# Optimization experiments

Hardware: AMD Instinct MI355X
Metric: run time of the kernel (lower is better)

The kernel has to match this reference:

```python
import jax, jax.numpy as jnp
import numpy as np

BUCKET = 64      # bucket_size
N_HASHES = 8
HEADS = 8
EMB = 256
DH = EMB // HEADS  # 32, per-head dim
SELF_ATTN_VAL = -5e4  # TOKEN_SELF_ATTN_VALUE in reformer-pytorch


def haar_dwt2_per(x):
    # one-level 2D haar DWT, periodization mode. x: [B,C,H,W] (H,W even)
    B, C, H, W = x.shape
    x = x.reshape(B, C, H // 2, 2, W // 2, 2)
    a = x[:, :, :, 0, :, 0]
    b = x[:, :, :, 0, :, 1]
    c = x[:, :, :, 1, :, 0]
    d = x[:, :, :, 1, :, 1]
    ll = (a + b + c + d) * 0.5
    lh = (a - b + c - d) * 0.5  # high-pass along W
    hl = (a + b - c - d) * 0.5  # high-pass along H
    hh = (a - b - c + d) * 0.5
    return ll, lh, hl, hh


def maxpool_3s2p1(x):
    # MaxPool2d(kernel=3, stride=2, padding=1)
    return jax.lax.reduce_window(x, -jnp.inf, jax.lax.max,
                                 (1, 1, 3, 3), (1, 1, 2, 2),
                                 ((0, 0), (0, 0), (1, 1), (1, 1)))


def _look_one_back(a):
    # concat each chunk with the previous chunk (wrap-around), along axis 2
    prev = jnp.concatenate([a[:, -1:], a[:, :-1]], axis=1)
    return jnp.concatenate([a, prev], axis=2)


def lsh_attention(qk, v, rotations):
    # qk, v: [bh, t, d]; rotations: [d, n_hashes, n_buckets//2]
    bh, t, d = qk.shape
    n_buckets = t // BUCKET
    # --- hash ---
    rotated = jnp.einsum('btf,fhi->bhti', qk, rotations)        # [bh,nh,t,nb/2]
    rotated = jnp.concatenate([rotated, -rotated], axis=-1)     # [bh,nh,t,nb]
    buckets = jnp.argmax(rotated, axis=-1)                      # [bh,nh,t]
    offsets = (jnp.arange(N_HASHES) * n_buckets)[None, :, None]
    buckets = (buckets + offsets).reshape(bh, -1)               # [bh, nh*t]
    # --- sort tokens by bucket ---
    ticker = jnp.arange(N_HASHES * t)
    bat = t * buckets + (ticker % t)[None, :]
    sticker = jnp.argsort(bat, axis=-1)                         # stable sort
    undo = jnp.argsort(sticker, axis=-1)
    st = sticker % t
    sqk = jnp.take_along_axis(qk, st[..., None], axis=1)
    sv = jnp.take_along_axis(v, st[..., None], axis=1)
    nc = N_HASHES * n_buckets
    bq_t = st.reshape(bh, nc, BUCKET)
    bqk = sqk.reshape(bh, nc, BUCKET, d)
    bv = sv.reshape(bh, nc, BUCKET, d)
    bq = bqk
    norm = jnp.linalg.norm(bqk, axis=-1, keepdims=True)
    bk = bqk / jnp.maximum(norm, 1e-6)                          # make_unit_length
    bk = _look_one_back(bk)
    bv = _look_one_back(bv)
    bkv_t = _look_one_back(bq_t[..., None])[..., 0]
    # --- bucketed attention ---
    dots = jnp.einsum('bnie,bnje->bnij', bq, bk) * (d ** -0.5)  # [bh,nc,64,128]
    self_mask = bq_t[:, :, :, None] == bkv_t[:, :, None, :]
    dots = jnp.where(self_mask, SELF_ATTN_VAL, dots)
    lse = jax.scipy.special.logsumexp(dots, axis=-1, keepdims=True)
    probs = jnp.exp(dots - lse)
    bo = jnp.einsum('bnij,bnje->bnie', probs, bv)
    so = bo.reshape(bh, -1, d)
    slog = lse.reshape(bh, -1)
    # --- unsort and combine hash rounds ---
    o = jnp.take_along_axis(so, undo[..., None], axis=1).reshape(bh, N_HASHES, t, d)
    logits = jnp.take_along_axis(slog, undo, axis=1).reshape(bh, N_HASHES, t, 1)
    w = jnp.exp(logits - jax.scipy.special.logsumexp(logits, axis=1, keepdims=True))
    return jnp.sum(o * w, axis=1)                               # [bh, t, d]


def setup_inputs() -> dict:
    key = jax.random.key(0)
    ks = jax.random.split(key, 6)
    B, C, H, W = 16, 128, 32, 32
    scale = 1.0 / np.sqrt(EMB)
    return {
        'x': jax.random.normal(ks[0], (B, C, H, W), dtype=jnp.float32),
        'w_qk': jax.random.normal(ks[1], (EMB, EMB), dtype=jnp.float32) * scale,
        'w_v': jax.random.normal(ks[2], (EMB, EMB), dtype=jnp.float32) * scale,
        'w_out': jax.random.normal(ks[3], (EMB, EMB), dtype=jnp.float32) * scale,
        'b_out': jnp.zeros((EMB,), dtype=jnp.float32),
        'rotations': jax.random.normal(ks[4], (DH, N_HASHES, 5), dtype=jnp.float32),
    }


def reference(x, w_qk, w_v, w_out, b_out, rotations):
    B = x.shape[0]
    x_spatial = maxpool_3s2p1(x)                      # [B,C,16,16]
    ll, lh, hl, hh = haar_dwt2_per(x)                 # each [B,C,16,16]
    xc = jnp.concatenate([x_spatial, ll, lh, hl, hh], axis=1)  # [B,5C,16,16]
    _, N, Hh, Ww = xc.shape
    tokens = xc.reshape(B, N, Hh * Ww)                # [B, 640, 256]
    qk = tokens @ w_qk
    v = tokens @ w_v
    qkh = qk.reshape(B, N, HEADS, DH).transpose(0, 2, 1, 3).reshape(B * HEADS, N, DH)
    vh = v.reshape(B, N, HEADS, DH).transpose(0, 2, 1, 3).reshape(B * HEADS, N, DH)
    o = lsh_attention(qkh, vh, rotations)
    o = o.reshape(B, HEADS, N, DH).transpose(0, 2, 1, 3).reshape(B, N, EMB)
    out = o @ w_out + b_out
    return out.reshape(B, N, Hh, Ww)
```

## Files before the change

kernel.cpp:

```cpp
#include <hip/hip_runtime.h>
#include <math.h>

#define B_     16
#define CIN_   128
#define NTOK_  640
#define PSP_   256
#define EMB_   256
#define HEADS_ 8
#define DH_    32
#define BH_    128
#define NH_    8
#define NBK_   10
#define NC_    80
#define TOTROWS_ 10240
#define SORTLEN_ 5120
#define VSTRIDE 136

typedef __attribute__((ext_vector_type(8))) short short8;
typedef __attribute__((ext_vector_type(4))) short short4v;
typedef __attribute__((ext_vector_type(4))) float f32x4;

__device__ __forceinline__ unsigned bf16r(float f) {
  return (__float_as_uint(f) + 0x8000u) >> 16;
}

__device__ __forceinline__ unsigned cvt_pk_bf16(float a, float b) {
  unsigned r;
  asm("v_cvt_pk_bf16_f32 %0, %1, %2" : "=v"(r) : "v"(a), "v"(b));
  return r;
}

__global__ __launch_bounds__(256) void k_tokens(const float* __restrict__ x,
                                                float* __restrict__ tok,
                                                const float* __restrict__ wv,
                                                const float* __restrict__ wo,
                                                unsigned short* __restrict__ wtv,
                                                unsigned short* __restrict__ wto) {
  if (blockIdx.x < 256) {
    int idx = blockIdx.x * 256 + threadIdx.x;
    int n = idx >> 8, k = idx & 255;
    wtv[idx] = (unsigned short)bf16r(wv[k * 256 + n]);
    wto[idx] = (unsigned short)bf16r(wo[k * 256 + n]);
  }
  int tid = blockIdx.x * 256 + threadIdx.x;
  int p  = tid & 255;
  int bc = tid >> 8;
  int i = p >> 4, j = p & 15;
  const float* xp = x + (size_t)bc * 1024;
  int r0 = i * 2, c0 = j * 2;

  float mx = -3.4e38f;
  #pragma unroll
  for (int dr = -1; dr <= 1; dr++) {
    int r = r0 + dr;
    if (r < 0 || r >= 32) continue;
    #pragma unroll
    for (int dc = -1; dc <= 1; dc++) {
      int cc = c0 + dc;
      if (cc < 0 || cc >= 32) continue;
      mx = fmaxf(mx, xp[r * 32 + cc]);
    }
  }
  float a  = xp[r0 * 32 + c0];
  float bv = xp[r0 * 32 + c0 + 1];
  float cv = xp[(r0 + 1) * 32 + c0];
  float dv = xp[(r0 + 1) * 32 + c0 + 1];
  float ll = (a + bv + cv + dv) * 0.5f;
  float lh = (a - bv + cv - dv) * 0.5f;
  float hl = (a + bv - cv - dv) * 0.5f;
  float hh = (a - bv - cv + dv) * 0.5f;

  int b = bc >> 7, c = bc & 127;
  float* tb = tok + (size_t)b * NTOK_ * PSP_ + p;
  tb[(size_t)(c      ) * PSP_] = mx;
  tb[(size_t)(c + 128) * PSP_] = ll;
  tb[(size_t)(c + 256) * PSP_] = lh;
  tb[(size_t)(c + 384) * PSP_] = hl;
  tb[(size_t)(c + 512) * PSP_] = hh;
}

__global__ __launch_bounds__(256) void k_gemm_qv(const float* __restrict__ A,
                                                 const float* __restrict__ Wq,
                                                 const unsigned short* __restrict__ WTv,
                                                 float* __restrict__ C,
                                                 unsigned short* __restrict__ Cb,
                                                 unsigned short* __restrict__ Cv) {
  __shared__ float As[64][68];
  __shared__ float Bs[64][64];
  int tid = threadIdx.x;

  if (blockIdx.x < 640) {
    int bx = blockIdx.x;
    int row0 = (bx >> 2) * 64, col0 = (bx & 3) * 64;
    int tx = tid & 15, ty = tid >> 4;
    float acc[4][4] = {};

    int lrow = tid >> 2, lkq = tid & 3;
    int bkr = tid >> 4, bcq = tid & 15;

    for (int k0 = 0; k0 < 256; k0 += 64) {
      float4 va[4], vb4[4];
      #pragma unroll
      for (int i = 0; i < 4; i++) {
        va[i]  = *(const float4*)(&A[(size_t)(row0 + lrow) * 256 + k0 + i * 16 + 4 * lkq]);
        vb4[i] = *(const float4*)(&Wq[(size_t)(k0 + i * 16 + bkr) * 256 + col0 + 4 * bcq]);
      }
      __syncthreads();
      #pragma unroll
      for (int i = 0; i < 4; i++) {
        As[i * 16 + 4 * lkq + 0][lrow] = va[i].x;
        As[i * 16 + 4 * lkq + 1][lrow] = va[i].y;
        As[i * 16 + 4 * lkq + 2][lrow] = va[i].z;
        As[i * 16 + 4 * lkq + 3][lrow] = va[i].w;
        *(float4*)(&Bs[i * 16 + bkr][4 * bcq]) = vb4[i];
      }
      __syncthreads();
      #pragma unroll
      for (int k = 0; k < 64; k++) {
        const float4 b4 = *(const float4*)(&Bs[k][4 * tx]);
        const float4 a4 = *(const float4*)(&As[k][4 * ty]);
        float ar[4] = {a4.x, a4.y, a4.z, a4.w};
        #pragma unroll
        for (int r = 0; r < 4; r++) {
          acc[r][0] += ar[r] * b4.x; acc[r][1] += ar[r] * b4.y;
          acc[r][2] += ar[r] * b4.z; acc[r][3] += ar[r] * b4.w;
        }
      }
    }
    #pragma unroll
    for (int r = 0; r < 4; r++) {
      float4 o;
      o.x = acc[r][0]; o.y = acc[r][1]; o.z = acc[r][2]; o.w = acc[r][3];
      size_t off = (size_t)(row0 + 4 * ty + r) * 256 + col0 + 4 * tx;
      *(float4*)(&C[off]) = o;
      uint2 ub;
      ub.x = bf16r(o.x) | (bf16r(o.y) << 16);
      ub.y = bf16r(o.z) | (bf16r(o.w) << 16);
      *(uint2*)(&Cb[off]) = ub;
    }
  } else {
    int vbk = blockIdx.x - 640;
    int wid = tid >> 6, lane = tid & 63;
    int lane15 = lane & 15, quad = lane >> 4;
    int row0 = (vbk >> 1) * 64 + wid * 16;
    int col0 = (vbk & 1) * 128;

    short8 fa[8];
    const float* arow = A + (size_t)(row0 + lane15) * 256;
    #pragma unroll
    for (int kc = 0; kc < 8; kc++) {
      float4 x0 = *(const float4*)(arow + kc * 32 + quad * 8);
      float4 x1 = *(const float4*)(arow + kc * 32 + quad * 8 + 4);
      short8 f;
      f[0] = (short)bf16r(x0.x); f[1] = (short)bf16r(x0.y);
      f[2] = (short)bf16r(x0.z); f[3] = (short)bf16r(x0.w);
      f[4] = (short)bf16r(x1.x); f[5] = (short)bf16r(x1.y);
      f[6] = (short)bf16r(x1.z); f[7] = (short)bf16r(x1.w);
      fa[kc] = f;
    }
    #pragma unroll
    for (int nt = 0; nt < 8; nt++) {
      int col = col0 + nt * 16 + lane15;
      f32x4 acc = {0.f, 0.f, 0.f, 0.f};
      const unsigned short* wrow = WTv + (size_t)col * 256;
      #pragma unroll
      for (int kc = 0; kc < 8; kc++) {
        short8 fb = *(const short8*)(wrow + kc * 32 + quad * 8);
        acc = __builtin_amdgcn_mfma_f32_16x16x32_bf16(fa[kc], fb, acc, 0, 0, 0);
      }
      #pragma unroll
      for (int rg = 0; rg < 4; rg++)
        Cv[(size_t)(row0 + 4 * quad + rg) * 256 + col] = (unsigned short)bf16r(acc[rg]);
    }
  }
}

__global__ __launch_bounds__(640) void k_sort(const float* __restrict__ qkg,
                                              const float* __restrict__ rot,
                                              int* __restrict__ st,
                                              float* __restrict__ nrmv) {
  int bh = blockIdx.x, h = blockIdx.y;
  int b = bh >> 3, head = bh & 7;
  __shared__ float srot[5][32];
  __shared__ int wcnt[10][10];
  __shared__ int woff[10][10];
  __shared__ int gbase[10];
  int tid = threadIdx.x, wv = tid >> 6, ln = tid & 63;

  if (tid < 160) {
    int i = tid >> 5, f = tid & 31;
    srot[i][f] = rot[f * (NH_ * 5) + h * 5 + i];
  }
  __syncthreads();

  int t = tid;
  const float* qr = qkg + ((size_t)b * NTOK_ + t) * EMB_ + head * DH_;
  float q[32];
  #pragma unroll
  for (int d4 = 0; d4 < 8; d4++) {
    float4 f = *(const float4*)(qr + d4 * 4);
    q[d4 * 4 + 0] = f.x; q[d4 * 4 + 1] = f.y; q[d4 * 4 + 2] = f.z; q[d4 * 4 + 3] = f.w;
  }
  if (h == 0) {
    float d2 = 0.f;
    #pragma unroll
    for (int dd = 0; dd < 32; dd++) d2 += q[dd] * q[dd];
    nrmv[(size_t)bh * NTOK_ + t] = sqrtf(d2);
  }
  float r[5];
  #pragma unroll
  for (int i = 0; i < 5; i++) {
    float d = 0.f;
    #pragma unroll
    for (int dd = 0; dd < 32; dd++) d += q[dd] * srot[i][dd];
    r[i] = d;
  }
  int bi = 0; float best = r[0];
  #pragma unroll
  for (int i = 1; i < 5; i++) if (r[i] > best) { best = r[i]; bi = i; }
  #pragma unroll
  for (int i = 0; i < 5; i++) if (-r[i] > best) { best = -r[i]; bi = 5 + i; }

  int myoff = 0;
  #pragma unroll
  for (int kb = 0; kb < 10; kb++) {
    unsigned long long mask = __ballot(bi == kb);
    if (ln == 0) wcnt[wv][kb] = (int)__popcll(mask);
    if (bi == kb) myoff = (int)__popcll(mask & ((1ull << ln) - 1ull));
  }
  __syncthreads();
  if (tid < 10) {
    int run = 0;
    #pragma unroll
    for (int w2 = 0; w2 < 10; w2++) { int tmp = wcnt[w2][tid]; woff[w2][tid] = run; run += tmp; }
    gbase[tid] = run;
  }
  __syncthreads();
  if (tid == 0) {
    int run = 0;
    #pragma unroll
    for (int kb = 0; kb < 10; kb++) { int tmp = gbase[kb]; gbase[kb] = run; run += tmp; }
  }
  __syncthreads();
  int rank = gbase[bi] + woff[wv][bi] + myoff;
  size_t gb = (size_t)bh * SORTLEN_ + (size_t)h * 640;
  st[gb + rank] = t;
}

__global__ __launch_bounds__(256) void k_attn(const unsigned short* __restrict__ qkb,
                                              const unsigned short* __restrict__ vb,
                                              const int* __restrict__ st,
                                              const float* __restrict__ nrmv,
                                              unsigned short* __restrict__ osort,
                                              float* __restrict__ lseg) {
  __shared__ __attribute__((aligned(16))) short sK[4096];
  __shared__ __attribute__((aligned(16))) short sVT[32 * VSTRIDE];
  __shared__ __attribute__((aligned(16))) short sP[2048];
  __shared__ float sM[64];
  __shared__ float sIK[128];
  __shared__ float sL[64];
  __shared__ int   stkv[128];

  const float scale = 0.17677669529663687f;
  const float LOG2E = 1.4426950408889634f;
  const float K2 = scale * LOG2E;
  int bh = blockIdx.x, c = blockIdx.y;
  int b = bh >> 3, head = bh & 7;
  int lane = threadIdx.x & 63, wid = threadIdx.x >> 6;
  size_t stb = (size_t)bh * SORTLEN_;
  int pcv = (c + NC_ - 1) % NC_;

  {
    int slot = threadIdx.x & 127;
    int hf   = threadIdx.x >> 7;
    int p0 = (slot < 64) ? (c * 64 + slot) : (pcv * 64 + (slot - 64));
    int t0 = st[stb + p0];
    size_t rowoff = ((size_t)(b * NTOK_ + t0)) * EMB_ + head * DH_;

    const uint4* kr = (const uint4*)(qkb + rowoff);
    uint4 ka = kr[2 * hf], kb2 = kr[2 * hf + 1];
    int pr = slot >> 1;
    int blk0 = ((slot & 1) << 2) | (2 * hf);
    *(uint4*)(&sK[pr * 64 + (((blk0    ) ^ (pr & 7)) << 3)]) = ka;
    *(uint4*)(&sK[pr * 64 + (((blk0 + 1) ^ (pr & 7)) << 3)]) = kb2;
    if (hf == 0) {
      stkv[slot] = t0;
      float nr = nrmv[(size_t)bh * NTOK_ + t0];
      if (slot < 64) sM[slot] = nr * scale;
      sIK[slot] = K2 / fmaxf(nr, 1e-6f);
    }

    const uint4* vr = (const uint4*)(vb + rowoff);
    uint4 va = vr[2 * hf], vb4 = vr[2 * hf + 1];
    unsigned uw[8] = {va.x, va.y, va.z, va.w, vb4.x, vb4.y, vb4.z, vb4.w};
    int vslot = (slot & 96) | (((slot & 15) >> 2) << 3) | (((slot >> 4) & 1) << 2) | (slot & 3);
    short* vbase = &sVT[hf * 16 * VSTRIDE + vslot];
    #pragma unroll
    for (int j = 0; j < 16; j++) {
      unsigned s = (j & 1) ? (uw[j >> 1] >> 16) : uw[j >> 1];
      vbase[j * VSTRIDE] = (short)s;
    }
  }
  __syncthreads();

  int lane15 = lane & 15, quad = lane >> 4;

  short8 fall[8];
  #pragma unroll
  for (int i = 0; i < 8; i++) {
    int key = 16 * i + lane15, pr = key >> 1;
    int blk = ((key & 1) << 2) | quad;
    fall[i] = *(const short8*)(&sK[pr * 64 + ((blk ^ (pr & 7)) << 3)]);
  }
  short8 fq;
  {
    int row = 16 * wid + lane15, pr = row >> 1;
    int blk = ((row & 1) << 2) | quad;
    fq = *(const short8*)(&sK[pr * 64 + ((blk ^ (pr & 7)) << 3)]);
  }

  int   tq  = stkv[16 * wid + lane15];
  float mq  = sM[16 * wid + lane15];
  float mq2 = mq * LOG2E;

  f32x4 O[2];
  #pragma unroll
  for (int vt = 0; vt < 2; vt++) { O[vt][0]=0.f; O[vt][1]=0.f; O[vt][2]=0.f; O[vt][3]=0.f; }
  float lacc = 0.f;

  #pragma unroll
  for (int s = 0; s < 4; s++) {
    f32x4 z = {0.f, 0.f, 0.f, 0.f};
    f32x4 Sv[2];
    #pragma unroll
    for (int ct = 0; ct < 2; ct++)
      Sv[ct] = __builtin_amdgcn_mfma_f32_16x16x32_bf16(fall[2 * s + ct], fq, z, 0, 0, 0);

    unsigned pk[2][2];
    #pragma unroll
    for (int ct = 0; ct < 2; ct++) {
      const int4   k4 = *(const int4*)(&stkv[32 * s + 16 * ct + 4 * quad]);
      const float4 c4 = *(const float4*)(&sIK[32 * s + 16 * ct + 4 * quad]);
      int   kk[4] = {k4.x, k4.y, k4.z, k4.w};
      float cc[4] = {c4.x, c4.y, c4.z, c4.w};
      float e[4];
      #pragma unroll
      for (int rg = 0; rg < 4; rg++) {
        float v = __builtin_exp2f(__builtin_fmaf(Sv[ct][rg], cc[rg], -mq2));
        if (kk[rg] == tq) v = 0.f;
        lacc += v;
        e[rg] = v;
      }
      pk[ct][0] = cvt_pk_bf16(e[0], e[1]);
      pk[ct][1] = cvt_pk_bf16(e[2], e[3]);
    }
    short8 fp;
    {
      union { unsigned u[4]; short8 v; } cv_;
      cv_.u[0] = pk[0][0]; cv_.u[1] = pk[0][1];
      cv_.u[2] = pk[1][0]; cv_.u[3] = pk[1][1];
      fp = cv_.v;
    }
    short8 fv[2];
    #pragma unroll
    for (int vt = 0; vt < 2; vt++)
      fv[vt] = *(const short8*)(&sVT[(16 * vt + lane15) * VSTRIDE + 32 * s + (quad << 3)]);
    #pragma unroll
    for (int vt = 0; vt < 2; vt++)
      O[vt] = __builtin_amdgcn_mfma_f32_16x16x32_bf16(fp, fv[vt], O[vt], 0, 0, 0);
  }

  lacc += __shfl_xor(lacc, 16);
  lacc += __shfl_xor(lacc, 32);

  int h = c / NBK_;
  if (lane < 16) {
    sL[16 * wid + lane] = lacc;
    lseg[((size_t)bh * NTOK_ + tq) * NH_ + h] = mq + __logf(lacc);
  }
  float4 lr = *(const float4*)(&sL[16 * wid + 4 * quad]);
  float lrow[4] = {lr.x, lr.y, lr.z, lr.w};
  #pragma unroll
  for (int rg = 0; rg < 4; rg++) {
    float invl = 1.f / lrow[rg];
    #pragma unroll
    for (int vt = 0; vt < 2; vt++) {
      float o = O[vt][rg] * invl;
      sP[(16 * wid + 4 * quad + rg) * 32 + 16 * vt + lane15] = (short)bf16r(o);
    }
  }
  __syncthreads();
  {
    int row = threadIdx.x >> 2, seg = threadIdx.x & 3;
    int t = stkv[row];
    uint4* dst = (uint4*)(osort + (((size_t)bh * NTOK_ + t) * NH_ + h) * 32 + seg * 8);
    *dst = ((const uint4*)sP)[threadIdx.x];
  }
}

__global__ __launch_bounds__(256) void k_combine(const unsigned short* __restrict__ osort,
                                                 const float* __restrict__ lseg,
                                                 unsigned short* __restrict__ cmb) {
  int g = blockIdx.x * 256 + threadIdx.x;
  int part = g & 3;
  int task = g >> 2;
  int bh = task / 640;
  int t  = task - bh * 640;
  size_t base = (size_t)task;

  float l[8];
  float4 l0 = *(const float4*)(lseg + base * 8);
  float4 l1 = *(const float4*)(lseg + base * 8 + 4);
  l[0]=l0.x; l[1]=l0.y; l[2]=l0.z; l[3]=l0.w;
  l[4]=l1.x; l[5]=l1.y; l[6]=l1.z; l[7]=l1.w;
  float m = -3.4e38f;
  #pragma unroll
  for (int h = 0; h < 8; h++) m = fmaxf(m, l[h]);
  float ssum = 0.f;
  #pragma unroll
  for (int h = 0; h < 8; h++) { l[h] = __expf(l[h] - m); ssum += l[h]; }
  float inv = 1.0f / ssum;

  float acc[8] = {};
  const uint4* orows = (const uint4*)osort;
  size_t obase = base * 32 + part;
  #pragma unroll
  for (int h = 0; h < 8; h++) {
    float w = l[h] * inv;
    uint4 u = orows[obase + h * 4];
    unsigned uu[4] = {u.x, u.y, u.z, u.w};
    #pragma unroll
    for (int q2 = 0; q2 < 4; q2++) {
      float lo = __uint_as_float(uu[q2] << 16);
      float hi = __uint_as_float(uu[q2] & 0xFFFF0000u);
      acc[q2 * 2 + 0] += w * lo;
      acc[q2 * 2 + 1] += w * hi;
    }
  }
  int b = bh >> 3, head = bh & 7;
  uint4 o;
  o.x = bf16r(acc[0]) | (bf16r(acc[1]) << 16);
  o.y = bf16r(acc[2]) | (bf16r(acc[3]) << 16);
  o.z = bf16r(acc[4]) | (bf16r(acc[5]) << 16);
  o.w = bf16r(acc[6]) | (bf16r(acc[7]) << 16);
  *(uint4*)(cmb + ((size_t)(b * NTOK_ + t)) * 256 + head * 32 + part * 8) = o;
}

__global__ __launch_bounds__(256) void k_oproj(const unsigned short* __restrict__ cmb,
                                               const unsigned short* __restrict__ WT,
                                               const float* __restrict__ bias,
                                               float* __restrict__ C) {
  int rt = blockIdx.x;
  int tid = threadIdx.x;
  int wid = tid >> 6, lane = tid & 63;
  int lane15 = lane & 15, quad = lane >> 4;
  int row0 = rt * 16;
  int col0 = wid * 64;

  short8 fa[8];
  const unsigned short* arow = cmb + (size_t)(row0 + lane15) * 256;
  #pragma unroll
  for (int kc = 0; kc < 8; kc++)
    fa[kc] = *(const short8*)(arow + kc * 32 + quad * 8);
  #pragma unroll
  for (int nt = 0; nt < 4; nt++) {
    int col = col0 + nt * 16 + lane15;
    f32x4 acc = {0.f, 0.f, 0.f, 0.f};
    const unsigned short* wrow = WT + (size_t)col * 256;
    #pragma unroll
    for (int kc = 0; kc < 8; kc++) {
      short8 fb = *(const short8*)(wrow + kc * 32 + quad * 8);
      acc = __builtin_amdgcn_mfma_f32_16x16x32_bf16(fa[kc], fb, acc, 0, 0, 0);
    }
    float bb = bias[col];
    #pragma unroll
    for (int rg = 0; rg < 4; rg++)
      C[(size_t)(row0 + 4 * quad + rg) * 256 + col] = acc[rg] + bb;
  }
}

extern "C" void kernel_launch(void* const* d_in, const int* in_sizes, int n_in,
                              void* d_out, int out_size, void* d_ws, size_t ws_size,
                              hipStream_t stream) {
  const float* x     = (const float*)d_in[0];
  const float* w_qk  = (const float*)d_in[1];
  const float* w_v   = (const float*)d_in[2];
  const float* w_out = (const float*)d_in[3];
  const float* b_out = (const float*)d_in[4];
  const float* rot   = (const float*)d_in[5];
  float* out = (float*)d_out;

  float* tokens  = (float*)d_ws;
  float* qk      = tokens + 2621440;
  unsigned short* qkb = (unsigned short*)(qk + 2621440);
  unsigned short* vbv = qkb + 2621440;
  int*   st      = (int*)(vbv + 2621440);
  float* lse     = (float*)(st + 655360);
  unsigned short* osort = (unsigned short*)(lse + 655360);
  unsigned short* wtv = osort + 20971520;
  unsigned short* wto = wtv + 65536;
  float* nrmv = tokens;
  unsigned short* cmb = (unsigned short*)qk;

  k_tokens<<<2048, 256, 0, stream>>>(x, tokens, w_v, w_out, wtv, wto);
  k_gemm_qv<<<960, 256, 0, stream>>>(tokens, w_qk, wtv, qk, qkb, vbv);
  k_sort<<<dim3(128, 8), 640, 0, stream>>>(qk, rot, st, nrmv);
  k_attn<<<dim3(128, 80), 256, 0, stream>>>(qkb, vbv, st, nrmv, osort, lse);
  k_combine<<<1280, 256, 0, stream>>>(osort, lse, cmb);
  k_oproj<<<640, 256, 0, stream>>>(cmb, wto, b_out, out);
}
```

Before: 199.4 us.

## Loop attention blocks over chunks per hash round, reusing previous chunk K/V

Each attention block now handles one (batch-head, hash round) pair and walks the 10 chunks in that round in sequence, instead of launching one block per chunk. K/V staging is double-buffered in shared memory, so the current chunk's keys and values are kept and reused as the look-back chunk in the next iteration, roughly halving gathered global loads. The self-token mask inside the current chunk is computed from position indices instead of token-id compares. The cost is a tenfold smaller grid with serial per-block work, which lowers available parallelism and latency hiding.

```diff
diff --git a/kernel.cpp b/kernel.cpp
--- a/kernel.cpp
+++ b/kernel.cpp
@@ -264,138 +264,148 @@
   const float scale = 0.17677669529663687f;
   const float LOG2E = 1.4426950408889634f;
   const float K2 = scale * LOG2E;
-  int bh = blockIdx.x, c = blockIdx.y;
+  int bh = blockIdx.x, h = blockIdx.y;
   int b = bh >> 3, head = bh & 7;
   int lane = threadIdx.x & 63, wid = threadIdx.x >> 6;
+  int lane15 = lane & 15, quad = lane >> 4;
   size_t stb = (size_t)bh * SORTLEN_;
-  int pcv = (c + NC_ - 1) % NC_;
-
-  {
-    int slot = threadIdx.x & 127;
-    int hf   = threadIdx.x >> 7;
-    int p0 = (slot < 64) ? (c * 64 + slot) : (pcv * 64 + (slot - 64));
-    int t0 = st[stb + p0];
-    size_t rowoff = ((size_t)(b * NTOK_ + t0)) * EMB_ + head * DH_;
-
-    const uint4* kr = (const uint4*)(qkb + rowoff);
-    uint4 ka = kr[2 * hf], kb2 = kr[2 * hf + 1];
-    int pr = slot >> 1;
-    int blk0 = ((slot & 1) << 2) | (2 * hf);
-    *(uint4*)(&sK[pr * 64 + (((blk0    ) ^ (pr & 7)) << 3)]) = ka;
-    *(uint4*)(&sK[pr * 64 + (((blk0 + 1) ^ (pr & 7)) << 3)]) = kb2;
-    if (hf == 0) {
-      stkv[slot] = t0;
-      float nr = nrmv[(size_t)bh * NTOK_ + t0];
-      if (slot < 64) sM[slot] = nr * scale;
-      sIK[slot] = K2 / fmaxf(nr, 1e-6f);
-    }
-
-    const uint4* vr = (const uint4*)(vb + rowoff);
-    uint4 va = vr[2 * hf], vb4 = vr[2 * hf + 1];
-    unsigned uw[8] = {va.x, va.y, va.z, va.w, vb4.x, vb4.y, vb4.z, vb4.w};
-    int vslot = (slot & 96) | (((slot & 15) >> 2) << 3) | (((slot >> 4) & 1) << 2) | (slot & 3);
-    short* vbase = &sVT[hf * 16 * VSTRIDE + vslot];
-    #pragma unroll
-    for (int j = 0; j < 16; j++) {
-      unsigned s = (j & 1) ? (uw[j >> 1] >> 16) : uw[j >> 1];
-      vbase[j * VSTRIDE] = (short)s;
-    }
-  }
-  __syncthreads();
-
-  int lane15 = lane & 15, quad = lane >> 4;
-
-  short8 fall[8];
-  #pragma unroll
-  for (int i = 0; i < 8; i++) {
-    int key = 16 * i + lane15, pr = key >> 1;
-    int blk = ((key & 1) << 2) | quad;
-    fall[i] = *(const short8*)(&sK[pr * 64 + ((blk ^ (pr & 7)) << 3)]);
-  }
-  short8 fq;
-  {
-    int row = 16 * wid + lane15, pr = row >> 1;
-    int blk = ((row & 1) << 2) | quad;
-    fq = *(const short8*)(&sK[pr * 64 + ((blk ^ (pr & 7)) << 3)]);
-  }
-
-  int   tq  = stkv[16 * wid + lane15];
-  float mq  = sM[16 * wid + lane15];
-  float mq2 = mq * LOG2E;
-
-  f32x4 O[2];
-  #pragma unroll
-  for (int vt = 0; vt < 2; vt++) { O[vt][0]=0.f; O[vt][1]=0.f; O[vt][2]=0.f; O[vt][3]=0.f; }
-  float lacc = 0.f;
-
-  #pragma unroll
-  for (int s = 0; s < 4; s++) {
-    f32x4 z = {0.f, 0.f, 0.f, 0.f};
-    f32x4 Sv[2];
-    #pragma unroll
-    for (int ct = 0; ct < 2; ct++)
-      Sv[ct] = __builtin_amdgcn_mfma_f32_16x16x32_bf16(fall[2 * s + ct], fq, z, 0, 0, 0);
-
-    unsigned pk[2][2];
-    #pragma unroll
-    for (int ct = 0; ct < 2; ct++) {
-      const int4   k4 = *(const int4*)(&stkv[32 * s + 16 * ct + 4 * quad]);
-      const float4 c4 = *(const float4*)(&sIK[32 * s + 16 * ct + 4 * quad]);
-      int   kk[4] = {k4.x, k4.y, k4.z, k4.w};
-      float cc[4] = {c4.x, c4.y, c4.z, c4.w};
-      float e[4];
-      #pragma unroll
-      for (int rg = 0; rg < 4; rg++) {
-        float v = __builtin_exp2f(__builtin_fmaf(Sv[ct][rg], cc[rg], -mq2));
-        if (kk[rg] == tq) v = 0.f;
-        lacc += v;
-        e[rg] = v;
-      }
-      pk[ct][0] = cvt_pk_bf16(e[0], e[1]);
-      pk[ct][1] = cvt_pk_bf16(e[2], e[3]);
-    }
-    short8 fp;
-    {
-      union { unsigned u[4]; short8 v; } cv_;
-      cv_.u[0] = pk[0][0]; cv_.u[1] = pk[0][1];
-      cv_.u[2] = pk[1][0]; cv_.u[3] = pk[1][1];
-      fp = cv_.v;
-    }
-    short8 fv[2];
-    #pragma unroll
-    for (int vt = 0; vt < 2; vt++)
-      fv[vt] = *(const short8*)(&sVT[(16 * vt + lane15) * VSTRIDE + 32 * s + (quad << 3)]);
-    #pragma unroll
-    for (int vt = 0; vt < 2; vt++)
-      O[vt] = __builtin_amdgcn_mfma_f32_16x16x32_bf16(fp, fv[vt], O[vt], 0, 0, 0);
-  }
-
-  lacc += __shfl_xor(lacc, 16);
-  lacc += __shfl_xor(lacc, 32);
-
-  int h = c / NBK_;
-  if (lane < 16) {
-    sL[16 * wid + lane] = lacc;
-    lseg[((size_t)bh * NTOK_ + tq) * NH_ + h] = mq + __logf(lacc);
-  }
-  float4 lr = *(const float4*)(&sL[16 * wid + 4 * quad]);
-  float lrow[4] = {lr.x, lr.y, lr.z, lr.w};
-  #pragma unroll
-  for (int rg = 0; rg < 4; rg++) {
-    float invl = 1.f / lrow[rg];
-    #pragma unroll
-    for (int vt = 0; vt < 2; vt++) {
-      float o = O[vt][rg] * invl;
-      sP[(16 * wid + 4 * quad + rg) * 32 + 16 * vt + lane15] = (short)bf16r(o);
-    }
-  }
-  __syncthreads();
-  {
-    int row = threadIdx.x >> 2, seg = threadIdx.x & 3;
-    int t = stkv[row];
-    uint4* dst = (uint4*)(osort + (((size_t)bh * NTOK_ + t) * NH_ + h) * 32 + seg * 8);
-    *dst = ((const uint4*)sP)[threadIdx.x];
-  }
+
+  int slot4 = threadIdx.x >> 2;
+  int qf    = threadIdx.x & 3;
+  int qd    = 16 * wid + lane15 - 4 * quad;
+
+#define STAGE(CC, HB, WRM)                                                    \
+  {                                                                           \
+    int t0 = st[stb + (CC) * 64 + slot4];                                     \
+    size_t rowoff = ((size_t)(b * NTOK_ + t0)) * EMB_ + head * DH_;           \
+    uint4 kq = ((const uint4*)(qkb + rowoff))[qf];                            \
+    int gs = (HB) * 64 + slot4;                                               \
+    int pr = gs >> 1;                                                         \
+    int blk = ((gs & 1) << 2) | qf;                                           \
+    *(uint4*)(&sK[pr * 64 + ((blk ^ (pr & 7)) << 3)]) = kq;                   \
+    uint4 vq = ((const uint4*)(vb + rowoff))[qf];                             \
+    int vloc = (slot4 & 32) | (((slot4 & 15) >> 2) << 3)                      \
+             | (((slot4 >> 4) & 1) << 2) | (slot4 & 3);                       \
+    short* vbase = &sVT[(qf * 8) * VSTRIDE + (HB) * 64 + vloc];               \
+    vbase[0 * VSTRIDE] = (short)(vq.x & 0xFFFFu);                             \
+    vbase[1 * VSTRIDE] = (short)(vq.x >> 16);                                 \
+    vbase[2 * VSTRIDE] = (short)(vq.y & 0xFFFFu);                             \
+    vbase[3 * VSTRIDE] = (short)(vq.y >> 16);                                 \
+    vbase[4 * VSTRIDE] = (short)(vq.z & 0xFFFFu);                             \
+    vbase[5 * VSTRIDE] = (short)(vq.z >> 16);                                 \
+    vbase[6 * VSTRIDE] = (short)(vq.w & 0xFFFFu);                             \
+    vbase[7 * VSTRIDE] = (short)(vq.w >> 16);                                 \
+    if (qf == 0) {                                                            \
+      stkv[gs] = t0;                                                          \
+      float nr = nrmv[(size_t)bh * NTOK_ + t0];                               \
+      sIK[gs] = K2 / fmaxf(nr, 1e-6f);                                        \
+      if (WRM) sM[slot4] = nr * scale;                                        \
+    }                                                                         \
+  }
+
+#define BODY(CI, CUR, PRV)                                                    \
+  {                                                                           \
+    STAGE(h * NBK_ + (CI), CUR, 1);                                           \
+    __syncthreads();                                                          \
+    short8 fall[8];                                                           \
+    _Pragma("unroll")                                                         \
+    for (int ii = 0; ii < 8; ii++) {                                          \
+      int hb = (ii < 4) ? (CUR) : (PRV);                                      \
+      int gs = hb * 64 + 16 * (ii & 3) + lane15;                              \
+      int pr = gs >> 1, blk = ((gs & 1) << 2) | quad;                         \
+      fall[ii] = *(const short8*)(&sK[pr * 64 + ((blk ^ (pr & 7)) << 3)]);    \
+    }                                                                         \
+    short8 fq;                                                                \
+    { int gs = (CUR) * 64 + 16 * wid + lane15;                                \
+      int pr = gs >> 1, blk = ((gs & 1) << 2) | quad;                         \
+      fq = *(const short8*)(&sK[pr * 64 + ((blk ^ (pr & 7)) << 3)]); }        \
+    int   tq  = stkv[(CUR) * 64 + 16 * wid + lane15];                         \
+    float mq  = sM[16 * wid + lane15];                                        \
+    float mq2 = mq * LOG2E;                                                   \
+    f32x4 O[2];                                                               \
+    O[0][0]=0.f; O[0][1]=0.f; O[0][2]=0.f; O[0][3]=0.f;                       \
+    O[1][0]=0.f; O[1][1]=0.f; O[1][2]=0.f; O[1][3]=0.f;                       \
+    float lacc = 0.f;                                                         \
+    _Pragma("unroll")                                                         \
+    for (int s = 0; s < 4; s++) {                                             \
+      int hb = (s < 2) ? (CUR) : (PRV);                                       \
+      int cb = hb * 64 + 32 * (s & 1);                                        \
+      f32x4 z = {0.f, 0.f, 0.f, 0.f};                                         \
+      f32x4 Sv[2];                                                            \
+      _Pragma("unroll")                                                       \
+      for (int ct = 0; ct < 2; ct++)                                          \
+        Sv[ct] = __builtin_amdgcn_mfma_f32_16x16x32_bf16(fall[2*s+ct], fq, z, 0, 0, 0); \
+      unsigned pk[2][2];                                                      \
+      _Pragma("unroll")                                                       \
+      for (int ct = 0; ct < 2; ct++) {                                        \
+        const float4 c4 = *(const float4*)(&sIK[cb + 16 * ct + 4 * quad]);    \
+        float cc[4] = {c4.x, c4.y, c4.z, c4.w};                               \
+        int kk[4];                                                            \
+        if (s >= 2) {                                                         \
+          const int4 k4 = *(const int4*)(&stkv[cb + 16 * ct + 4 * quad]);     \
+          kk[0] = k4.x; kk[1] = k4.y; kk[2] = k4.z; kk[3] = k4.w;             \
+        }                                                                     \
+        float e[4];                                                           \
+        _Pragma("unroll")                                                     \
+        for (int rg = 0; rg < 4; rg++) {                                      \
+          float v = __builtin_exp2f(__builtin_fmaf(Sv[ct][rg], cc[rg], -mq2)); \
+          if (s < 2) {                                                        \
+            if (qd == 32 * s + 16 * ct + rg) v = 0.f;                         \
+          } else {                                                            \
+            if (kk[rg] == tq) v = 0.f;                                        \
+          }                                                                   \
+          lacc += v;                                                          \
+          e[rg] = v;                                                          \
+        }                                                                     \
+        pk[ct][0] = cvt_pk_bf16(e[0], e[1]);                                  \
+        pk[ct][1] = cvt_pk_bf16(e[2], e[3]);                                  \
+      }                                                                       \
+      short8 fp;                                                              \
+      { union { unsigned u[4]; short8 v; } cv_;                               \
+        cv_.u[0] = pk[0][0]; cv_.u[1] = pk[0][1];                             \
+        cv_.u[2] = pk[1][0]; cv_.u[3] = pk[1][1];                             \
+        fp = cv_.v; }                                                         \
+      short8 fv[2];                                                           \
+      _Pragma("unroll")                                                       \
+      for (int vt = 0; vt < 2; vt++)                                          \
+        fv[vt] = *(const short8*)(&sVT[(16 * vt + lane15) * VSTRIDE + cb + (quad << 3)]); \
+      _Pragma("unroll")                                                       \
+      for (int vt = 0; vt < 2; vt++)                                          \
+        O[vt] = __builtin_amdgcn_mfma_f32_16x16x32_bf16(fp, fv[vt], O[vt], 0, 0, 0); \
+    }                                                                         \
+    lacc += __shfl_xor(lacc, 16);                                             \
+    lacc += __shfl_xor(lacc, 32);                                             \
+    if (lane < 16) {                                                          \
+      sL[16 * wid + lane] = lacc;                                             \
+      lseg[((size_t)bh * NTOK_ + tq) * NH_ + h] = mq + __logf(lacc);          \
+    }                                                                         \
+    float4 lr = *(const float4*)(&sL[16 * wid + 4 * quad]);                   \
+    float lrow[4] = {lr.x, lr.y, lr.z, lr.w};                                 \
+    _Pragma("unroll")                                                         \
+    for (int rg = 0; rg < 4; rg++) {                                          \
+      float invl = 1.f / lrow[rg];                                            \
+      _Pragma("unroll")                                                       \
+      for (int vt = 0; vt < 2; vt++) {                                        \
+        float o = O[vt][rg] * invl;                                           \
+        sP[(16 * wid + 4 * quad + rg) * 32 + 16 * vt + lane15] = (short)bf16r(o); \
+      }                                                                       \
+    }                                                                         \
+    __syncthreads();                                                          \
+    { int row = threadIdx.x >> 2, seg = threadIdx.x & 3;                      \
+      int t = stkv[(CUR) * 64 + row];                                         \
+      uint4* dst = (uint4*)(osort + (((size_t)bh * NTOK_ + t) * NH_ + h) * 32 + seg * 8); \
+      *dst = ((const uint4*)sP)[threadIdx.x]; }                               \
+  }
+
+  int pro = (h * NBK_ + NC_ - 1) % NC_;
+  STAGE(pro, 1, 0);
+
+  for (int i2 = 0; i2 < NBK_ / 2; i2++) {
+    BODY(2 * i2,     0, 1);
+    BODY(2 * i2 + 1, 1, 0);
+  }
+#undef BODY
+#undef STAGE
 }
 
 __global__ __launch_bounds__(256) void k_combine(const unsigned short* __restrict__ osort,
@@ -505,7 +515,7 @@
   k_tokens<<<2048, 256, 0, stream>>>(x, tokens, w_v, w_out, wtv, wto);
   k_gemm_qv<<<960, 256, 0, stream>>>(tokens, w_qk, wtv, qk, qkb, vbv);
   k_sort<<<dim3(128, 8), 640, 0, stream>>>(qk, rot, st, nrmv);
-  k_attn<<<dim3(128, 80), 256, 0, stream>>>(qkb, vbv, st, nrmv, osort, lse);
+  k_attn<<<dim3(128, 8), 256, 0, stream>>>(qkb, vbv, st, nrmv, osort, lse);
   k_combine<<<1280, 256, 0, stream>>>(osort, lse, cmb);
   k_oproj<<<640, 256, 0, stream>>>(cmb, wto, b_out, out);
 }
```

After: 207.2 us. 1.04x slower.
